# Kernel optimization log

Measured on AMD Instinct MI355X. Metric: run time of the kernel, lower is better.

The kernel has to match this reference:

```python
import jax, jax.numpy as jnp
import numpy as np

B, T, C, H = 4, 1024, 2048, 16
HD = C // H          # head dim = 128 (even, as RoPE requires)
BLOCK = 1024         # config.block_size == config.max_block_size
NEG = -1e30          # finite stand-in for -inf in the additive attention bias


def setup_inputs() -> dict:
    key = jax.random.key(0)
    k1, k2, k3, k4, k5 = jax.random.split(key, 5)
    x = jax.random.normal(k1, (B, T, C), jnp.float32)
    cumulative_scores = jax.random.uniform(k2, (B, T), jnp.float32)  # kept small: fed to exp()
    token_index = jax.random.randint(k3, (B, T), 0, BLOCK, dtype=jnp.int32)
    padding_mask = jnp.ones((B, T), jnp.int32)
    # xavier-ish scale so softmax doesn't saturate
    W_attn = jax.random.normal(k4, (C, 3 * C), jnp.float32) / np.sqrt(C)
    W_proj = jax.random.normal(k5, (C, C), jnp.float32) / np.sqrt(C)
    return dict(x=x, cumulative_scores=cumulative_scores, token_index=token_index,
                padding_mask=padding_mask, W_attn=W_attn, W_proj=W_proj)


def _rotate_half(a):
    a1, a2 = a[..., : HD // 2], a[..., HD // 2:]
    return jnp.concatenate([-a2, a1], axis=-1)


def reference(x, cumulative_scores, token_index, padding_mask, W_attn, W_proj):
    # QKV projection (bias=False per config)
    qkv = x @ W_attn                                  # (B,T,3C)
    q, k, v = jnp.split(qkv, 3, axis=2)
    heads = lambda a: a.reshape(B, T, H, HD).transpose(0, 2, 1, 3)  # (B,H,T,HD)
    q, k, v = heads(q), heads(k), heads(v)

    # input-dependent partial rotation positions (exact replica of the original
    # scatter: token_index (B,T) fancy-indexes the last axis of a (B,BLOCK)
    # buffer, so counts are summed over ALL batch rows, as in the source)
    counts = jnp.zeros((B, BLOCK), jnp.float32).at[..., token_index].add(1.0)
    t = jnp.cumsum(jnp.take_along_axis(1.0 / (counts + 1e-10), token_index, axis=-1), axis=-1)  # (B,T)

    # RoPE with per-token positions t (seq_dim=-2, offset 0 for both q and k)
    inv_freq = 1.0 / (10000.0 ** (jnp.arange(0, HD, 2, dtype=jnp.float32) / HD))
    freqs = jnp.einsum('bt,j->btj', t, inv_freq)
    emb = jnp.concatenate([freqs, freqs], axis=-1)[:, None, :, :]   # (B,1,T,HD)
    sin, cos = jnp.sin(emb), jnp.cos(emb)
    q = q * cos + _rotate_half(q) * sin
    k = k * cos + _rotate_half(k) * sin

    # 'fork' plan overrides on the last rotary channel
    q = q.at[..., -1].set(1.0)
    k = k.at[..., -1].set(jnp.broadcast_to(cumulative_scores[:, None, :], (B, H, T)))

    # V rescaled by exp(cumulative_scores)
    v = v * jnp.exp(cumulative_scores)[:, None, :, None]

    # causal + key-padding additive bias, SDPA with scale 1/sqrt(HD)
    keep = jnp.tril(jnp.ones((T, T), bool))[None, None] & padding_mask.astype(bool)[:, None, None, :]
    scores = jnp.einsum('bhqd,bhkd->bhqk', q, k) / np.sqrt(HD)
    scores = jnp.where(keep, scores, NEG)
    attn = jax.nn.softmax(scores, axis=-1)
    y = jnp.einsum('bhqk,bhkd->bhqd', attn, v)

    y = y.transpose(0, 2, 1, 3).reshape(B, T, C)
    return y @ W_proj
```

## Files before the change

kernel.cpp:

```cpp
#include <hip/hip_runtime.h>

#define BB 4
#define TT 1024
#define CCH 2048
#define HH 16
#define HDIM 128
#define NBLK 1024
#define MM (BB*TT)
#define N1 (3*CCH)
#define NQT 16

typedef _Float16 f16;
typedef _Float16 half8 __attribute__((ext_vector_type(8)));
typedef _Float16 half4 __attribute__((ext_vector_type(4)));
typedef float floatx4 __attribute__((ext_vector_type(4)));

__device__ __forceinline__ void g2lds16(const void* g, void* l) {
    __builtin_amdgcn_global_load_lds((const __attribute__((address_space(1))) void*)g,
                                     (__attribute__((address_space(3))) void*)l, 16, 0, 0);
}

__global__ void k_prep(const float* __restrict__ Wa, const float* __restrict__ Wp,
                       const float* __restrict__ x,
                       f16* __restrict__ WaT, f16* __restrict__ WpT,
                       f16* __restrict__ x16) {
    int z = blockIdx.z;
    if (z == 2) {
        int i = (blockIdx.y * 192 + blockIdx.x) * 256 + threadIdx.x + threadIdx.y * 32;
        if (i >= MM * CCH / 4) return;
        float4 v = ((const float4*)x)[i];
        union { ushort4 u; f16 h[4]; } o;
        o.h[0] = (f16)v.x; o.h[1] = (f16)v.y; o.h[2] = (f16)v.z; o.h[3] = (f16)v.w;
        ((ushort4*)x16)[i] = o.u;
        return;
    }
    const float* in = (z == 0) ? Wa : Wp;
    f16* out = (z == 0) ? WaT : WpT;
    int Cc = (z == 0) ? N1 : CCH;
    if (blockIdx.x * 32 >= Cc) return;
    __shared__ float tile[32][33];
    int c0 = blockIdx.x * 32, r0 = blockIdx.y * 32;
    int tx = threadIdx.x, ty = threadIdx.y;
#pragma unroll
    for (int k = 0; k < 4; k++) {
        int r = ty + k * 8;
        tile[r][tx] = in[(size_t)(r0 + r) * Cc + c0 + tx];
    }
    __syncthreads();
#pragma unroll
    for (int k = 0; k < 4; k++) {
        int r = ty + k * 8;
        out[(size_t)(c0 + r) * CCH + r0 + tx] = (f16)tile[tx][r];
    }
}

__global__ void k_trv(const f16* __restrict__ in, f16* __restrict__ out) {
    __shared__ f16 tile[32][34];
    int bh = blockIdx.z;
    int h0 = blockIdx.x * 32, t0 = blockIdx.y * 32;
    int tx = threadIdx.x, ty = threadIdx.y;
#pragma unroll
    for (int k = 0; k < 4; k++) {
        int t = ty + k * 8;
        tile[t][tx] = in[((size_t)bh * TT + t0 + t) * HDIM + h0 + tx];
    }
    __syncthreads();
#pragma unroll
    for (int k = 0; k < 4; k++) {
        int r = ty + k * 8;
        out[((size_t)bh * HDIM + h0 + r) * TT + t0 + tx] = tile[tx][r];
    }
}

__global__ void k_hist(const int* __restrict__ tok, int* __restrict__ cnt) {
    int i = blockIdx.x * blockDim.x + threadIdx.x;
    if (i < MM) atomicAdd(cnt + tok[i], 1);
}

__global__ __launch_bounds__(1024) void k_scan(const int* __restrict__ tok,
                                               const int* __restrict__ cnt,
                                               const int* __restrict__ pm,
                                               float* __restrict__ tpos,
                                               float* __restrict__ pb) {
    __shared__ float s[TT];
    int b = blockIdx.x, t = threadIdx.x;
    s[t] = 1.0f / ((float)cnt[tok[b * TT + t]] + 1e-10f);
    __syncthreads();
    for (int off = 1; off < TT; off <<= 1) {
        float add = (t >= off) ? s[t - off] : 0.0f;
        __syncthreads();
        s[t] += add;
        __syncthreads();
    }
    tpos[b * TT + t] = s[t];
    pb[b * TT + t] = pm[b * TT + t] ? 0.0f : -1e30f;
}

__global__ void k_rope(const float* __restrict__ tpos, float2* __restrict__ tab) {
    int i = blockIdx.x * 256 + threadIdx.x;
    int row = i >> 6, j = i & 63;
    float f = tpos[row] * expf((float)j * -0.14391156929f);
    float sn, cn; sincosf(f, &sn, &cn);
    tab[i] = make_float2(cn, sn);
}

#define BAR() __builtin_amdgcn_s_barrier()
#define RDA(S, base, ck) do { _Pragma("unroll") for (int m_ = 0; m_ < 4; m_++) \
    S[m_] = *(const half8*)((base) + aoffb + (m_ << 11) + (ck)); } while (0)
#define RDB(S, base, ck) do { _Pragma("unroll") for (int n_ = 0; n_ < 4; n_++) \
    S[n_] = *(const half8*)((base) + bofs[n_] + (ck)); } while (0)
#define STAGEA(t, base) do { _Pragma("unroll") for (int k_ = 0; k_ < 4; k_++) \
    g2lds16(Ab + (size_t)(k_ * 64) * 2048 + ((t) << 6) + srcr, \
            (base) + (w * 8 + k_ * 64) * 128); } while (0)
#define STAGEB(t, base) do { _Pragma("unroll") for (int k_ = 0; k_ < 2; k_++) \
    g2lds16(Bb + (size_t)(k_ * 64) * 2048 + ((t) << 6) + srcr, \
            (base) + (w * 8 + k_ * 64) * 128); } while (0)
#define MF16(SA, SB) do { _Pragma("unroll") for (int m_ = 0; m_ < 4; m_++) \
    _Pragma("unroll") for (int n_ = 0; n_ < 4; n_++) \
    acc[m_][n_] = __builtin_amdgcn_mfma_f32_16x16x32_f16(SA[m_], SB[n_], acc[m_][n_], 0, 0, 0); } while (0)

template <int MODE>
__global__ __launch_bounds__(512, 2) void k_gemm8(const f16* __restrict__ A,
                                                  const f16* __restrict__ Bt,
                                                  float* __restrict__ Cp,
                                                  const float2* __restrict__ tab,
                                                  const float* __restrict__ cs,
                                                  f16* __restrict__ qr,
                                                  f16* __restrict__ kr,
                                                  f16* __restrict__ vsc) {
    const float SCALE = 0.08838834764831845f;
    const int NBN = MODE ? 48 : 16;
    const int NWG = MODE ? 768 : 256;
    const int CPX = NWG >> 3;
    __shared__ __align__(16) f16 As[3 * 16384];
    __shared__ __align__(16) f16 Bs[3 * 8192];

    int bid = blockIdx.x;
    int s = (bid & 7) * CPX + (bid >> 3);
    int bm = s / NBN, bn = s % NBN;

    int tid = threadIdx.x;
    int w = tid >> 6, lane = tid & 63, quad = lane >> 4, l16 = lane & 15;
    int wm = w & 3, wn = w >> 2;

    const f16* Ab = A + (size_t)(bm << 8) * 2048;
    const f16* Bb = Bt + (size_t)(bn << 7) * 2048;

    int rl = lane >> 3, cl = lane & 7;
    int gl = (cl - rl) & 7;
    int srcr = (w * 8 + rl) * 2048 + gl * 8;

    const int aoffb = (wm * 64 + l16) << 7;
    const int bofs[4] = { (wn * 32 + l16) << 7,        (wn * 32 + 64 + l16) << 7,
                          (wn * 32 + 16 + l16) << 7,   (wn * 32 + 80 + l16) << 7 };
    const int ck0 = ((quad + l16) & 7) << 4;
    const int ck1 = ck0 ^ 64;

    floatx4 acc[4][4];
#pragma unroll
    for (int i = 0; i < 4; i++)
#pragma unroll
        for (int j = 0; j < 4; j++) acc[i][j] = (floatx4){0.f, 0.f, 0.f, 0.f};

    half8 S0a[4], S1a[4];
    half8 S0b[4], S1b[4];

    char* a0 = (char*)As; char* a1 = a0 + 32768; char* a2 = a0 + 65536;
    char* b0 = (char*)Bs; char* b1 = b0 + 16384; char* b2 = b0 + 32768;

    STAGEA(0, a0); STAGEB(0, b0);
    STAGEA(1, a1); STAGEB(1, b1);
    asm volatile("s_waitcnt vmcnt(6)" ::: "memory");
    BAR();
    RDA(S0a, a0, ck0); RDB(S0b, b0, ck0);

#pragma unroll 1
    for (int t = 0; t < 32; ++t) {
        RDA(S1a, a0, ck1); RDB(S1b, b0, ck1);
        if (t + 2 < 32) { STAGEA(t + 2, a2); STAGEB(t + 2, b2); }
        __builtin_amdgcn_s_setprio(1); MF16(S0a, S0b); __builtin_amdgcn_s_setprio(0);
        if (t < 30) { asm volatile("s_waitcnt vmcnt(6)" ::: "memory"); }
        else        { asm volatile("s_waitcnt vmcnt(0)" ::: "memory"); }
        BAR();
        if (t < 31) { RDA(S0a, a1, ck0); RDB(S0b, b1, ck0); }
        __builtin_amdgcn_s_setprio(1); MF16(S1a, S1b); __builtin_amdgcn_s_setprio(0);
        BAR();
        char* ta = a0; a0 = a1; a1 = a2; a2 = ta;
        char* tb = b0; b0 = b1; b1 = b2; b2 = tb;
    }

    if (MODE == 0) {
#pragma unroll
        for (int mf = 0; mf < 4; mf++)
#pragma unroll
            for (int nf = 0; nf < 4; nf++) {
                int col = (bn << 7) + ((nf & 1) << 6) + wn * 32 + ((nf >> 1) << 4) + l16;
#pragma unroll
                for (int r = 0; r < 4; r++) {
                    int row = (bm << 8) + wm * 64 + mf * 16 + (quad << 2) + r;
                    Cp[(size_t)row * CCH + col] = acc[mf][nf][r];
                }
            }
    } else {
        int type = bn >> 4;
        int h = bn & 15;
        if (type < 2) {
            f16* outp = (type == 0) ? qr : kr;
#pragma unroll
            for (int mf = 0; mf < 4; mf++)
#pragma unroll
                for (int r = 0; r < 4; r++) {
                    int row = (bm << 8) + wm * 64 + mf * 16 + (quad << 2) + r;
#pragma unroll
                    for (int p = 0; p < 2; p++) {
                        int d1 = wn * 32 + p * 16 + l16;
                        float2 tc = tab[row * 64 + d1];
                        float a1v = acc[mf][2 * p][r], a2v = acc[mf][2 * p + 1][r];
                        float o1 = a1v * tc.x - a2v * tc.y;
                        float o2 = a2v * tc.x + a1v * tc.y;
                        if (type == 0) {
                            if (d1 == 63) o2 = 1.0f;
                            o1 *= SCALE; o2 *= SCALE;
                        } else {
                            if (d1 == 63) o2 = cs[row];
                        }
                        size_t ob = ((size_t)((row >> 10) * HH + h) * TT + (row & 1023)) * HDIM + d1;
                        outp[ob] = (f16)o1;
                        outp[ob + 64] = (f16)o2;
                    }
                }
        } else {
#pragma unroll
            for (int mf = 0; mf < 4; mf++)
#pragma unroll
                for (int r = 0; r < 4; r++) {
                    int row = (bm << 8) + wm * 64 + mf * 16 + (quad << 2) + r;
                    float ve = __expf(cs[row]);
#pragma unroll
                    for (int nf = 0; nf < 4; nf++) {
                        int d = ((nf & 1) << 6) + wn * 32 + ((nf >> 1) << 4) + l16;
                        size_t ob = ((size_t)((row >> 10) * HH + h) * TT + (row & 1023)) * HDIM + d;
                        vsc[ob] = (f16)(acc[mf][nf][r] * ve);
                    }
                }
        }
    }
}

__global__ __launch_bounds__(256) void k_attn(const f16* __restrict__ qr,
                                              const f16* __restrict__ kr,
                                              const f16* __restrict__ vt,
                                              const float* __restrict__ pb,
                                              f16* __restrict__ y) {
    __shared__ __align__(16) f16 Ks[2][64 * 136];
    __shared__ __align__(16) f16 Vs[2][128 * 72];
    __shared__ float pbs[2][64];
    int p = blockIdx.x & (NQT / 2 - 1);
    int bh = blockIdx.x >> 3;
    int b = bh >> 4, h = bh & 15;
    int tid = threadIdx.x;
    int w = tid >> 6, lane = tid & 63, quad = lane >> 4, l16 = lane & 15;
    const int krow0 = tid >> 4, kcol0 = (tid & 15) << 3;
    const int vrow0 = tid >> 3, vcol0 = (tid & 7) << 3;
#pragma unroll
    for (int pass = 0; pass < 2; pass++) {
        int qt = pass ? (NQT - 1 - p) : p;
        int q0 = qt << 6;
        int qg = q0 + w * 16 + l16;
        const f16* Qp = qr + ((size_t)bh * TT + qg) * HDIM;
        half8 qf[4];
#pragma unroll
        for (int kc = 0; kc < 4; kc++) qf[kc] = *(const half8*)&Qp[kc * 32 + (quad << 3)];
        floatx4 O[8];
#pragma unroll
        for (int i = 0; i < 8; i++) O[i] = (floatx4){0.f, 0.f, 0.f, 0.f};
        float mx = -1e30f, ls = 0.f;
        {
            const f16* Kb = kr + (size_t)bh * TT * HDIM;
            const f16* Vb = vt + (size_t)bh * HDIM * TT;
#pragma unroll
            for (int i = 0; i < 4; i++) {
                *(uint4*)&Ks[0][(krow0 + i * 16) * 136 + kcol0] =
                    *(const uint4*)&Kb[(size_t)(krow0 + i * 16) * HDIM + kcol0];
                *(uint4*)&Vs[0][(vrow0 + i * 32) * 72 + vcol0] =
                    *(const uint4*)&Vb[(size_t)(vrow0 + i * 32) * TT + vcol0];
            }
            if (tid < 64) pbs[0][tid] = pb[b * TT + tid];
        }
        __syncthreads();
        int cur = 0;
        for (int kt = 0; kt <= qt; kt++) {
            uint4 kreg[4], vreg[4];
            float pbnext = 0.f;
            const bool have = (kt < qt);
            if (have) {
                const f16* Kb = kr + ((size_t)bh * TT + ((kt + 1) << 6)) * HDIM;
                const f16* Vb = vt + (size_t)bh * HDIM * TT + ((kt + 1) << 6);
#pragma unroll
                for (int i = 0; i < 4; i++) {
                    kreg[i] = *(const uint4*)&Kb[(size_t)(krow0 + i * 16) * HDIM + kcol0];
                    vreg[i] = *(const uint4*)&Vb[(size_t)(vrow0 + i * 32) * TT + vcol0];
                }
                if (tid < 64) pbnext = pb[b * TT + ((kt + 1) << 6) + tid];
            }
            const f16* Kl = Ks[cur];
            const f16* Vl = Vs[cur];
            floatx4 Sv[4];
#pragma unroll
            for (int mc = 0; mc < 4; mc++) Sv[mc] = (floatx4){0.f, 0.f, 0.f, 0.f};
#pragma unroll
            for (int kc = 0; kc < 4; kc++)
#pragma unroll
                for (int mc = 0; mc < 4; mc++) {
                    half8 kf = *(const half8*)&Kl[(mc * 16 + l16) * 136 + kc * 32 + (quad << 3)];
                    Sv[mc] = __builtin_amdgcn_mfma_f32_16x16x32_f16(kf, qf[kc], Sv[mc], 0, 0, 0);
                }
            float pv[4][4];
            float mnew = mx;
            if (kt == qt) {
#pragma unroll
                for (int mc = 0; mc < 4; mc++) {
                    float4 pbv = *(const float4*)&pbs[cur][mc * 16 + (quad << 2)];
#pragma unroll
                    for (int i = 0; i < 4; i++) {
                        int kv = (kt << 6) + mc * 16 + (quad << 2) + i;
                        float s = (kv <= qg) ? Sv[mc][i] + ((const float*)&pbv)[i] : -1e30f;
                        pv[mc][i] = s;
                        mnew = fmaxf(mnew, s);
                    }
                }
            } else {
#pragma unroll
                for (int mc = 0; mc < 4; mc++) {
                    float4 pbv = *(const float4*)&pbs[cur][mc * 16 + (quad << 2)];
#pragma unroll
                    for (int i = 0; i < 4; i++) {
                        float s = Sv[mc][i] + ((const float*)&pbv)[i];
                        pv[mc][i] = s;
                        mnew = fmaxf(mnew, s);
                    }
                }
            }
            mnew = fmaxf(mnew, __shfl_xor(mnew, 16));
            mnew = fmaxf(mnew, __shfl_xor(mnew, 32));
            float al = __expf(mx - mnew);
            mx = mnew;
            float psum = 0.f;
#pragma unroll
            for (int mc = 0; mc < 4; mc++)
#pragma unroll
                for (int i = 0; i < 4; i++) {
                    float e = __expf(pv[mc][i] - mnew);
                    pv[mc][i] = e;
                    psum += e;
                }
            psum += __shfl_xor(psum, 16);
            psum += __shfl_xor(psum, 32);
            ls = ls * al + psum;
#pragma unroll
            for (int hm = 0; hm < 8; hm++)
#pragma unroll
                for (int i = 0; i < 4; i++) O[hm][i] *= al;
            half4 pf[4];
#pragma unroll
            for (int mc = 0; mc < 4; mc++) {
                pf[mc][0] = (f16)pv[mc][0]; pf[mc][1] = (f16)pv[mc][1];
                pf[mc][2] = (f16)pv[mc][2]; pf[mc][3] = (f16)pv[mc][3];
            }
#pragma unroll
            for (int mc = 0; mc < 4; mc++)
#pragma unroll
                for (int hm = 0; hm < 8; hm++) {
                    half4 vf = *(const half4*)&Vl[(hm * 16 + l16) * 72 + mc * 16 + (quad << 2)];
                    O[hm] = __builtin_amdgcn_mfma_f32_16x16x16f16(vf, pf[mc], O[hm], 0, 0, 0);
                }
            if (have) {
                int nxt = cur ^ 1;
#pragma unroll
                for (int i = 0; i < 4; i++) {
                    *(uint4*)&Ks[nxt][(krow0 + i * 16) * 136 + kcol0] = kreg[i];
                    *(uint4*)&Vs[nxt][(vrow0 + i * 32) * 72 + vcol0] = vreg[i];
                }
                if (tid < 64) pbs[nxt][tid] = pbnext;
            }
            __syncthreads();
            cur ^= 1;
        }
        float inv = 1.0f / ls;
#pragma unroll
        for (int hm = 0; hm < 8; hm++) {
            half4 ov;
#pragma unroll
            for (int i = 0; i < 4; i++) ov[i] = (f16)(O[hm][i] * inv);
            *(half4*)&y[((size_t)b * TT + qg) * CCH + h * HDIM + hm * 16 + (quad << 2)] = ov;
        }
        __syncthreads();
    }
}

extern "C" void kernel_launch(void* const* d_in, const int* in_sizes, int n_in,
                              void* d_out, int out_size, void* d_ws, size_t ws_size,
                              hipStream_t stream) {
    const float* x   = (const float*)d_in[0];
    const float* cs  = (const float*)d_in[1];
    const int*   tok = (const int*)d_in[2];
    const int*   pm  = (const int*)d_in[3];
    const float* Wa  = (const float*)d_in[4];
    const float* Wp  = (const float*)d_in[5];
    float* out = (float*)d_out;
    char* ws = (char*)d_ws;

    f16* x16 = (f16*)(ws + 0);
    f16* WaT = (f16*)(ws + 16777216);
    f16* vt  = (f16*)(ws + 41943040);
    f16* WpT = (f16*)(ws + 58720256);
    float2* tab = (float2*)(ws + 67108864);
    f16* qr  = (f16*)(ws + 92274688);
    f16* kr  = (f16*)(ws + 109051904);
    f16* vsc = (f16*)(ws + 125829120);
    int*   cnt  = (int*)(ws + 142606336);
    float* tpos = (float*)(ws + 142610432);
    float* pb   = (float*)(ws + 142626816);
    f16* y   = x16;

    hipMemsetAsync(cnt, 0, NBLK * sizeof(int), stream);
    k_hist<<<MM / 256, 256, 0, stream>>>(tok, cnt);
    k_scan<<<BB, TT, 0, stream>>>(tok, cnt, pm, tpos, pb);
    k_rope<<<MM * 64 / 256, 256, 0, stream>>>(tpos, tab);
    k_prep<<<dim3(N1 / 32, CCH / 32, 3), dim3(32, 8), 0, stream>>>(Wa, Wp, x, WaT, WpT, x16);
    k_gemm8<1><<<768, 512, 0, stream>>>(x16, WaT, nullptr, tab, cs, qr, kr, vsc);
    k_trv<<<dim3(4, 32, BB * HH), dim3(32, 8), 0, stream>>>(vsc, vt);
    k_attn<<<BB * HH * (NQT / 2), 256, 0, stream>>>(qr, kr, vt, pb, y);
    k_gemm8<0><<<256, 512, 0, stream>>>(y, WpT, out, nullptr, nullptr, nullptr, nullptr, nullptr);
}
```

Baseline: 371.1 us.

## Write V transposed from QKV GEMM epilogue and widen weight-transpose tiles

The QKV GEMM epilogue now writes the exp-scaled V straight into the transposed (head-dim by time) layout using 4-wide half stores. This removes the separate V transpose kernel and its round trip through global memory. The weight prep kernel now converts to f16 while loading, uses 64-row tiles with paired-half stores, and halves the grid, so the x conversion loop covers two elements per thread. Stores in the epilogue are now strided by T across d, which could reduce write coalescing.

```diff
diff --git a/kernel.cpp b/kernel.cpp
--- a/kernel.cpp
+++ b/kernel.cpp
@@ -25,50 +25,40 @@
                        f16* __restrict__ WaT, f16* __restrict__ WpT,
                        f16* __restrict__ x16) {
     int z = blockIdx.z;
+    int tx = threadIdx.x, ty = threadIdx.y;
     if (z == 2) {
-        int i = (blockIdx.y * 192 + blockIdx.x) * 256 + threadIdx.x + threadIdx.y * 32;
-        if (i >= MM * CCH / 4) return;
-        float4 v = ((const float4*)x)[i];
-        union { ushort4 u; f16 h[4]; } o;
-        o.h[0] = (f16)v.x; o.h[1] = (f16)v.y; o.h[2] = (f16)v.z; o.h[3] = (f16)v.w;
-        ((ushort4*)x16)[i] = o.u;
+        int base = (blockIdx.y * 192 + blockIdx.x) * 256 + ty * 32 + tx;
+#pragma unroll
+        for (int q = 0; q < 2; q++) {
+            int i = base + q * (192 * 32 * 256);
+            if (i < MM * CCH / 4) {
+                float4 v = ((const float4*)x)[i];
+                union { ushort4 u; f16 h[4]; } o;
+                o.h[0] = (f16)v.x; o.h[1] = (f16)v.y; o.h[2] = (f16)v.z; o.h[3] = (f16)v.w;
+                ((ushort4*)x16)[i] = o.u;
+            }
+        }
         return;
     }
     const float* in = (z == 0) ? Wa : Wp;
     f16* out = (z == 0) ? WaT : WpT;
     int Cc = (z == 0) ? N1 : CCH;
     if (blockIdx.x * 32 >= Cc) return;
-    __shared__ float tile[32][33];
-    int c0 = blockIdx.x * 32, r0 = blockIdx.y * 32;
-    int tx = threadIdx.x, ty = threadIdx.y;
+    __shared__ f16 tile[64][34];
+    int c0 = blockIdx.x * 32, r0 = blockIdx.y * 64;
+#pragma unroll
+    for (int k = 0; k < 8; k++) {
+        int r = ty + k * 8;
+        tile[r][tx] = (f16)in[(size_t)(r0 + r) * Cc + c0 + tx];
+    }
+    __syncthreads();
 #pragma unroll
     for (int k = 0; k < 4; k++) {
-        int r = ty + k * 8;
-        tile[r][tx] = in[(size_t)(r0 + r) * Cc + c0 + tx];
-    }
-    __syncthreads();
-#pragma unroll
-    for (int k = 0; k < 4; k++) {
-        int r = ty + k * 8;
-        out[(size_t)(c0 + r) * CCH + r0 + tx] = (f16)tile[tx][r];
-    }
-}
-
-__global__ void k_trv(const f16* __restrict__ in, f16* __restrict__ out) {
-    __shared__ f16 tile[32][34];
-    int bh = blockIdx.z;
-    int h0 = blockIdx.x * 32, t0 = blockIdx.y * 32;
-    int tx = threadIdx.x, ty = threadIdx.y;
-#pragma unroll
-    for (int k = 0; k < 4; k++) {
-        int t = ty + k * 8;
-        tile[t][tx] = in[((size_t)bh * TT + t0 + t) * HDIM + h0 + tx];
-    }
-    __syncthreads();
-#pragma unroll
-    for (int k = 0; k < 4; k++) {
-        int r = ty + k * 8;
-        out[((size_t)bh * HDIM + h0 + r) * TT + t0 + tx] = tile[tx][r];
+        int c = ty + k * 8;
+        union { ushort2 u; f16 h[2]; } o2;
+        o2.h[0] = tile[2 * tx][c];
+        o2.h[1] = tile[2 * tx + 1][c];
+        *(ushort2*)&out[(size_t)(c0 + c) * CCH + r0 + 2 * tx] = o2.u;
     }
 }
 
@@ -231,18 +221,23 @@
                 }
         } else {
 #pragma unroll
-            for (int mf = 0; mf < 4; mf++)
-#pragma unroll
-                for (int r = 0; r < 4; r++) {
-                    int row = (bm << 8) + wm * 64 + mf * 16 + (quad << 2) + r;
-                    float ve = __expf(cs[row]);
-#pragma unroll
-                    for (int nf = 0; nf < 4; nf++) {
-                        int d = ((nf & 1) << 6) + wn * 32 + ((nf >> 1) << 4) + l16;
-                        size_t ob = ((size_t)((row >> 10) * HH + h) * TT + (row & 1023)) * HDIM + d;
-                        vsc[ob] = (f16)(acc[mf][nf][r] * ve);
-                    }
-                }
+            for (int mf = 0; mf < 4; mf++) {
+                int row0 = (bm << 8) + wm * 64 + mf * 16 + (quad << 2);
+                float4 cs4 = *(const float4*)&cs[row0];
+                float ve[4];
+                ve[0] = __expf(cs4.x); ve[1] = __expf(cs4.y);
+                ve[2] = __expf(cs4.z); ve[3] = __expf(cs4.w);
+                size_t bhbase = (size_t)((row0 >> 10) * HH + h) * HDIM;
+                int t0 = row0 & 1023;
+#pragma unroll
+                for (int nf = 0; nf < 4; nf++) {
+                    int d = ((nf & 1) << 6) + wn * 32 + ((nf >> 1) << 4) + l16;
+                    half4 ov;
+#pragma unroll
+                    for (int r = 0; r < 4; r++) ov[r] = (f16)(acc[mf][nf][r] * ve[r]);
+                    *(half4*)&vsc[(bhbase + d) * TT + t0] = ov;
+                }
+            }
         }
     }
 }
@@ -417,7 +412,6 @@
     float2* tab = (float2*)(ws + 67108864);
     f16* qr  = (f16*)(ws + 92274688);
     f16* kr  = (f16*)(ws + 109051904);
-    f16* vsc = (f16*)(ws + 125829120);
     int*   cnt  = (int*)(ws + 142606336);
     float* tpos = (float*)(ws + 142610432);
     float* pb   = (float*)(ws + 142626816);
@@ -427,9 +421,8 @@
     k_hist<<<MM / 256, 256, 0, stream>>>(tok, cnt);
     k_scan<<<BB, TT, 0, stream>>>(tok, cnt, pm, tpos, pb);
     k_rope<<<MM * 64 / 256, 256, 0, stream>>>(tpos, tab);
-    k_prep<<<dim3(N1 / 32, CCH / 32, 3), dim3(32, 8), 0, stream>>>(Wa, Wp, x, WaT, WpT, x16);
-    k_gemm8<1><<<768, 512, 0, stream>>>(x16, WaT, nullptr, tab, cs, qr, kr, vsc);
-    k_trv<<<dim3(4, 32, BB * HH), dim3(32, 8), 0, stream>>>(vsc, vt);
+    k_prep<<<dim3(192, 32, 3), dim3(32, 8), 0, stream>>>(Wa, Wp, x, WaT, WpT, x16);
+    k_gemm8<1><<<768, 512, 0, stream>>>(x16, WaT, nullptr, tab, cs, qr, kr, vt);
     k_attn<<<BB * HH * (NQT / 2), 256, 0, stream>>>(qr, kr, vt, pb, y);
     k_gemm8<0><<<256, 512, 0, stream>>>(y, WpT, out, nullptr, nullptr, nullptr, nullptr, nullptr);
 }
```

Measured after the change: 364.8 us. About the same (-1.7%).
